# Kernel tuning notes

Hardware: AMD Instinct MI355X
Metric: run time of the kernel (lower is better)

## Reference

```python
import jax, jax.numpy as jnp
import numpy as np
import math

B, SQ, SK = 8, 1024, 1024
DQ = DK = DV = 1024
H = 16
EPS = 1e-5


def _layer_norm(x, g, b):
    mu = jnp.mean(x, axis=-1, keepdims=True)
    var = jnp.mean(jnp.square(x - mu), axis=-1, keepdims=True)
    return (x - mu) * jax.lax.rsqrt(var + EPS) * g + b


def setup_inputs() -> dict:
    key = jax.random.key(0)
    ks = jax.random.split(key, 8)
    s_q = 1.0 / math.sqrt(DQ)
    s_v = 1.0 / math.sqrt(DV)
    return {
        "Q": jax.random.normal(ks[0], (B, SQ, DQ), dtype=jnp.float32),
        "K": jax.random.normal(ks[1], (B, SK, DK), dtype=jnp.float32),
        "Wq": jax.random.normal(ks[2], (DQ, DV), dtype=jnp.float32) * s_q,
        "bq": jnp.zeros((DV,), dtype=jnp.float32),
        "Wk": jax.random.normal(ks[3], (DK, DV), dtype=jnp.float32) * s_q,
        "bk": jnp.zeros((DV,), dtype=jnp.float32),
        "Wv": jax.random.normal(ks[4], (DK, DV), dtype=jnp.float32) * s_q,
        "bv": jnp.zeros((DV,), dtype=jnp.float32),
        "Wo": jax.random.normal(ks[5], (DV, DV), dtype=jnp.float32) * s_v,
        "bo": jnp.zeros((DV,), dtype=jnp.float32),
        "g0": jnp.ones((DV,), dtype=jnp.float32),
        "b0": jnp.zeros((DV,), dtype=jnp.float32),
        "g1": jnp.ones((DV,), dtype=jnp.float32),
        "b1": jnp.zeros((DV,), dtype=jnp.float32),
    }


def reference(Q, K, Wq, bq, Wk, bk, Wv, bv, Wo, bo, g0, b0, g1, b1):
    dh = DV // H
    q = Q @ Wq + bq                      # [B,SQ,DV]
    k = K @ Wk + bk                      # [B,SK,DV]
    v = K @ Wv + bv                      # [B,SK,DV]
    # split/cat over heads == reshape to [B,S,H,dh]
    qh = q.reshape(B, SQ, H, dh)
    kh = k.reshape(B, SK, H, dh)
    vh = v.reshape(B, SK, H, dh)
    # NOTE: original scales by sqrt(dim_V), not sqrt(head_dim)
    scores = jnp.einsum("bqhd,bkhd->bhqk", qh, kh) / math.sqrt(DV)
    A = jax.nn.softmax(scores, axis=-1)  # [B,H,SQ,SK]
    attn = jnp.einsum("bhqk,bkhd->bqhd", A, vh)
    out = q + attn.reshape(B, SQ, DV)    # residual with projected Q
    out = _layer_norm(out, g0, b0)
    out = out + jax.nn.relu(out @ Wo + bo)
    out = _layer_norm(out, g1, b1)
    return out
```

## Files before the change

kernel.cpp:

```cpp
#include <hip/hip_runtime.h>
#include <hip/hip_bf16.h>
#include <stdint.h>

#define NB 8
#define NSQ 1024
#define NSK 1024
#define ND 1024
#define NH 16
#define NDH 64
#define NM (NB * NSQ)
#define LOG2E 1.4426950408889634f

typedef __bf16 bf16;
typedef __bf16 bf16x8 __attribute__((ext_vector_type(8)));
typedef float f32x4 __attribute__((ext_vector_type(4)));
typedef float f32x16 __attribute__((ext_vector_type(16)));
typedef unsigned int uint32;

__device__ __forceinline__ void async_load16(const void* g, void* l) {
  __builtin_amdgcn_global_load_lds(
      (__attribute__((address_space(1))) void*)g,
      (__attribute__((address_space(3))) void*)l, 16, 0, 0);
}

__device__ __forceinline__ void permswap(uint32& x, uint32& y) {
#if __has_builtin(__builtin_amdgcn_permlane32_swap)
  auto r = __builtin_amdgcn_permlane32_swap(x, y, false, false);
  x = r[0]; y = r[1];
#else
  asm volatile("v_permlane32_swap_b32 %0, %1" : "+v"(x), "+v"(y));
#endif
}

__global__ __launch_bounds__(256) void transpose_cvt4(
    const float* __restrict__ W0, const float* __restrict__ W1,
    const float* __restrict__ W2, const float* __restrict__ W3,
    bf16* __restrict__ O0, bf16* __restrict__ O1,
    bf16* __restrict__ O2, bf16* __restrict__ O3) {
  const float* W; bf16* Wt;
  switch (blockIdx.z) {
    case 0: W = W0; Wt = O0; break;
    case 1: W = W1; Wt = O1; break;
    case 2: W = W2; Wt = O2; break;
    default: W = W3; Wt = O3; break;
  }
  __shared__ float t[64][65];
  const int bc = blockIdx.x * 64;
  const int br = blockIdx.y * 64;
  const int tid = threadIdx.x;
  for (int c = tid; c < 1024; c += 256) {
    int r = c >> 4, off = (c & 15) * 4;
    float4 v = *(const float4*)&W[(size_t)(br + r) * 1024 + bc + off];
    t[r][off] = v.x; t[r][off + 1] = v.y; t[r][off + 2] = v.z; t[r][off + 3] = v.w;
  }
  __syncthreads();
  for (int c = tid; c < 512; c += 256) {
    int cc = c >> 3, rr = (c & 7) * 8;
    union { uint4 u; bf16 h[8]; } o;
#pragma unroll
    for (int i = 0; i < 8; ++i) o.h[i] = (bf16)t[rr + i][cc];
    *(uint4*)&Wt[(size_t)(bc + cc) * 1024 + br + rr] = o.u;
  }
}

__global__ __launch_bounds__(256) void transpose_v(const bf16* __restrict__ vsrc,
                                                   bf16* __restrict__ vT) {
  const int st = blockIdx.x * 64;
  const int bh = blockIdx.y;
  const int b = bh >> 4, h = bh & 15;
  __shared__ __align__(16) bf16 t[64][72];
  const int tid = threadIdx.x;
  for (int c = tid; c < 512; c += 256) {
    int s = c >> 3, off = (c & 7) * 8;
    *(uint4*)&t[s][off] =
        *(const uint4*)&vsrc[(size_t)(b * NSK + st + s) * 2048 + 1024 + h * NDH + off];
  }
  __syncthreads();
  for (int c = tid; c < 512; c += 256) {
    int d = c >> 3, s0 = (c & 7) * 8;
    union { uint4 u; bf16 h[8]; } o;
#pragma unroll
    for (int i = 0; i < 8; ++i) o.h[i] = t[s0 + i][d];
    *(uint4*)&vT[((size_t)(bh * NDH + d)) * NSK + st + s0] = o.u;
  }
}

template <int BM, int MODE, int NXC, bool AF32>
__global__ __launch_bounds__(256, 2) void gemm3b(
    const float* __restrict__ Af, const bf16* __restrict__ Ab,
    const bf16* __restrict__ Bt,
    const float* __restrict__ bias, const float* __restrict__ bias2,
    bf16* __restrict__ Cb, const bf16* __restrict__ Resb, float scale, int N) {
  constexpr int NT = 32;
  constexpr int AR = BM / 64;
  constexpr int MR = BM / 32;
  __shared__ __align__(16) bf16 Asl[3][BM * 32];
  __shared__ __align__(16) bf16 Bsl[3][128 * 32];

  const int tid = threadIdx.x;
  const int flat = blockIdx.x;
  const int xi = (flat & 7) * 64 + (flat >> 3);
  const int bcol = (xi & (NXC - 1)) * 128;
  const int brow = (xi / NXC) * BM;

  const int w = tid >> 6, lane = tid & 63;
  const int wm = w >> 1, wn = w & 1;
  const int lr = lane & 15, l4 = lane >> 4;
  const int rgrp = l4 * 4;
  const int gph = (l4 ^ ((lr >> 1) & 3)) * 8;

  const int srow = tid >> 2;
  const int gsrc = (tid & 3) ^ ((tid >> 3) & 3);
  const bf16* Bg = Bt + (size_t)(bcol + srow) * 1024 + gsrc * 8;
  const int ldo = srow * 32 + (tid & 3) * 8;

  auto stageB = [&](int d, int kt) {
#pragma unroll
    for (int r = 0; r < 2; ++r)
      async_load16(Bg + (size_t)r * (64 * 1024) + kt * 32, &Bsl[d][r * 2048 + ldo]);
  };
  auto stageA_lds = [&](int d, int kt) {
#pragma unroll
    for (int r = 0; r < AR; ++r)
      async_load16(Ab + (size_t)(brow + srow + r * 64) * 1024 + gsrc * 8 + kt * 32,
                   &Asl[d][r * 2048 + ldo]);
  };

  float4 areg[AR][2];
  auto issueA = [&](int kt) {
    const float* base = Af + (size_t)(brow + srow) * 1024 + gsrc * 8 + kt * 32;
#pragma unroll
    for (int r = 0; r < AR; ++r) {
      areg[r][0] = *(const float4*)(base + (size_t)r * (64 * 1024));
      areg[r][1] = *(const float4*)(base + (size_t)r * (64 * 1024) + 4);
    }
  };
  auto writeA = [&](int d) {
#pragma unroll
    for (int r = 0; r < AR; ++r) {
      bf16x8 o;
      o[0] = (bf16)areg[r][0].x; o[1] = (bf16)areg[r][0].y;
      o[2] = (bf16)areg[r][0].z; o[3] = (bf16)areg[r][0].w;
      o[4] = (bf16)areg[r][1].x; o[5] = (bf16)areg[r][1].y;
      o[6] = (bf16)areg[r][1].z; o[7] = (bf16)areg[r][1].w;
      *(bf16x8*)&Asl[d][r * 2048 + ldo] = o;
    }
  };
  auto wait_vm_steady = [&]() {
    if constexpr (AF32) {
      if constexpr (BM == 256) asm volatile("s_waitcnt vmcnt(10)" ::: "memory");
      else                     asm volatile("s_waitcnt vmcnt(6)" ::: "memory");
    } else {
      if constexpr (BM == 256) asm volatile("s_waitcnt vmcnt(6)" ::: "memory");
      else                     asm volatile("s_waitcnt vmcnt(4)" ::: "memory");
    }
  };

  f32x4 acc[MR][4] = {};

  if constexpr (AF32) {
    issueA(0); stageB(0, 0);
    writeA(0);
    issueA(1); stageB(1, 1);
    wait_vm_steady();
    asm volatile("s_waitcnt lgkmcnt(0)" ::: "memory");
  } else {
    stageA_lds(0, 0); stageB(0, 0);
    stageA_lds(1, 1); stageB(1, 1);
    wait_vm_steady();
  }
  __builtin_amdgcn_s_barrier();

  int cur = 0, st2 = 2;
  for (int t = 0; t < NT; ++t) {
    bf16x8 af[MR], bfr[4];
#pragma unroll
    for (int i = 0; i < MR; ++i)
      af[i] = *(const bf16x8*)&Asl[cur][(wm * (BM / 2) + i * 16 + lr) * 32 + gph];
#pragma unroll
    for (int n = 0; n < 4; ++n)
      bfr[n] = *(const bf16x8*)&Bsl[cur][(wn * 64 + n * 16 + lr) * 32 + gph];
    if constexpr (AF32) {
      if (t + 1 < NT) writeA((cur == 2) ? 0 : cur + 1);
      if (t + 2 < NT) { issueA(t + 2); stageB(st2, t + 2); }
    } else {
      if (t + 2 < NT) { stageA_lds(st2, t + 2); stageB(st2, t + 2); }
    }
    __builtin_amdgcn_s_setprio(1);
#pragma unroll
    for (int i = 0; i < MR; ++i)
#pragma unroll
      for (int n = 0; n < 4; ++n)
        acc[i][n] = __builtin_amdgcn_mfma_f32_16x16x32_bf16(af[i], bfr[n], acc[i][n], 0, 0, 0);
    __builtin_amdgcn_s_setprio(0);
    if (t + 2 < NT)      wait_vm_steady();
    else if (t + 1 < NT) asm volatile("s_waitcnt vmcnt(0)" ::: "memory");
    asm volatile("s_waitcnt lgkmcnt(0)" ::: "memory");
    __builtin_amdgcn_s_barrier();
    cur = (cur == 2) ? 0 : cur + 1;
    st2 = (st2 == 2) ? 0 : st2 + 1;
  }

#pragma unroll
  for (int m = 0; m < MR; ++m) {
#pragma unroll
    for (int n = 0; n < 4; ++n) {
      const int col = bcol + wn * 64 + n * 16 + lr;
      float bv, sc;
      if (MODE == 2) {
        const bool isV = (bcol >= 1024);
        bv = isV ? bias2[col - 1024] : bias[col];
        sc = isV ? 1.0f : LOG2E;
      } else {
        bv = bias[col];
        sc = scale;
      }
#pragma unroll
      for (int r = 0; r < 4; ++r) {
        const int row = brow + wm * (BM / 2) + m * 16 + rgrp + r;
        float v = acc[m][n][r] + bv;
        if (MODE == 1) {
          float res = (float)Resb[(size_t)row * N + col];
          Cb[(size_t)row * N + col] = (bf16)(res + (v > 0.f ? v : 0.f));
        } else {
          Cb[(size_t)row * N + col] = (bf16)(v * sc);
        }
      }
    }
  }
}

__global__ __launch_bounds__(512, 4) void attn_kernel(
    const bf16* __restrict__ qb, const bf16* __restrict__ kvb,
    const bf16* __restrict__ vT, bf16* __restrict__ attnout) {
  const int bh = blockIdx.y;
  const int b = bh >> 4, h = bh & 15;
  const int tid = threadIdx.x, w = tid >> 6, lane = tid & 63;
  const int l31 = lane & 31;
  const int l1 = lane >> 5;
  const int q0w = blockIdx.x * 256 + w * 32;

  __shared__ __align__(16) bf16 Kl[2][64 * 64];
  __shared__ __align__(16) bf16 Vl[2][64 * 64];

  const int srow = tid >> 3;
  const int sgran = tid & 7;
  const int gsw = sgran ^ (srow & 7);
  const int ldst = srow * 64 + sgran * 8;
  const int rg = l31 & 7;

  const bf16* kbase = kvb + (size_t)(b * NSK) * 2048 + h * NDH;
  const bf16* vbase = vT + (size_t)(bh * NDH) * NSK;

  bf16x8 qf[4];
#pragma unroll
  for (int kd = 0; kd < 4; ++kd)
    qf[kd] = *(const bf16x8*)&qb[(size_t)(b * NSQ + q0w + l31) * ND +
                                 h * NDH + kd * 16 + l1 * 8];

  f32x16 oacc0 = {}, oacc1 = {}, lacc = {};
  bf16x8 ones;
#pragma unroll
  for (int i = 0; i < 8; ++i) ones[i] = (bf16)1.0f;

  auto stage = [&](int bi, int kt) {
    async_load16(kbase + (size_t)(kt + srow) * 2048 + gsw * 8, &Kl[bi][ldst]);
    async_load16(vbase + (size_t)srow * NSK + kt + gsw * 8, &Vl[bi][ldst]);
  };

  stage(0, 0);

  for (int t = 0; t < 16; ++t) {
    const int bi = t & 1;
    asm volatile("s_waitcnt vmcnt(0)" ::: "memory");
    __syncthreads();
    if (t < 15) stage(bi ^ 1, (t + 1) * 64);

    uint32 W[2][4][2];
#pragma unroll
    for (int n = 0; n < 2; ++n) {
      f32x16 s = {};
      __builtin_amdgcn_s_setprio(1);
#pragma unroll
      for (int kd = 0; kd < 4; ++kd) {
        bf16x8 kf = *(const bf16x8*)&Kl[bi][(n * 32 + l31) * 64 + (((kd * 2 + l1) ^ rg) * 8)];
        s = __builtin_amdgcn_mfma_f32_32x32x16_bf16(kf, qf[kd], s, 0, 0, 0);
      }
      __builtin_amdgcn_s_setprio(0);
#pragma unroll
      for (int r2 = 0; r2 < 4; ++r2)
#pragma unroll
        for (int p = 0; p < 2; ++p) {
          float elo = __builtin_amdgcn_exp2f(s[r2 * 4 + 2 * p]);
          float ehi = __builtin_amdgcn_exp2f(s[r2 * 4 + 2 * p + 1]);
          uint32 wd;
          asm("v_cvt_pk_bf16_f32 %0, %1, %2" : "=v"(wd) : "v"(elo), "v"(ehi));
          W[n][r2][p] = wd;
        }
    }
    __builtin_amdgcn_s_setprio(1);
#pragma unroll
    for (int kc = 0; kc < 4; ++kc) {
      uint32 x0 = W[kc >> 1][(kc & 1) * 2][0], y0 = W[kc >> 1][(kc & 1) * 2 + 1][0];
      uint32 x1 = W[kc >> 1][(kc & 1) * 2][1], y1 = W[kc >> 1][(kc & 1) * 2 + 1][1];
      permswap(x0, y0);
      permswap(x1, y1);
      union { uint32 u[4]; bf16x8 v; } cvt;
      cvt.u[0] = x0; cvt.u[1] = x1; cvt.u[2] = y0; cvt.u[3] = y1;
      bf16x8 pa = cvt.v;
      bf16x8 vf0 = *(const bf16x8*)&Vl[bi][(l31) * 64 + (((kc * 2 + l1) ^ rg) * 8)];
      bf16x8 vf1 = *(const bf16x8*)&Vl[bi][(32 + l31) * 64 + (((kc * 2 + l1) ^ rg) * 8)];
      oacc0 = __builtin_amdgcn_mfma_f32_32x32x16_bf16(pa, vf0, oacc0, 0, 0, 0);
      oacc1 = __builtin_amdgcn_mfma_f32_32x32x16_bf16(pa, vf1, oacc1, 0, 0, 0);
      lacc = __builtin_amdgcn_mfma_f32_32x32x16_bf16(pa, ones, lacc, 0, 0, 0);
    }
    __builtin_amdgcn_s_setprio(0);
  }

  float inv[16];
#pragma unroll
  for (int r = 0; r < 16; ++r) inv[r] = 1.0f / lacc[r];
#pragma unroll
  for (int r = 0; r < 16; ++r) {
    const int row = q0w + (r & 3) + 8 * (r >> 2) + 4 * l1;
    attnout[(size_t)(b * NSQ + row) * ND + h * NDH + l31] = (bf16)(oacc0[r] * inv[r]);
    attnout[(size_t)(b * NSQ + row) * ND + h * NDH + 32 + l31] = (bf16)(oacc1[r] * inv[r]);
  }
}

template <bool RES, bool OUTF>
__global__ __launch_bounds__(256) void ln_kernel(
    const bf16* __restrict__ x, const bf16* __restrict__ rq, float rscale,
    const float* __restrict__ g, const float* __restrict__ be,
    bf16* __restrict__ yb, float* __restrict__ yf) {
  __shared__ float sm[4];
  const int row = blockIdx.x, tid = threadIdx.x;
  const size_t base = (size_t)row * ND + tid * 4;
  union { uint2 u; bf16 h[4]; } xv;
  xv.u = *(const uint2*)(x + base);
  float v0 = (float)xv.h[0], v1 = (float)xv.h[1], v2 = (float)xv.h[2], v3 = (float)xv.h[3];
  if (RES) {
    union { uint2 u; bf16 h[4]; } q;
    q.u = *(const uint2*)(rq + base);
    v0 += rscale * (float)q.h[0]; v1 += rscale * (float)q.h[1];
    v2 += rscale * (float)q.h[2]; v3 += rscale * (float)q.h[3];
  }
  float s = v0 + v1 + v2 + v3;
#pragma unroll
  for (int off = 32; off > 0; off >>= 1) s += __shfl_down(s, off, 64);
  if ((tid & 63) == 0) sm[tid >> 6] = s;
  __syncthreads();
  const float mean = (sm[0] + sm[1] + sm[2] + sm[3]) * (1.0f / ND);
  __syncthreads();
  const float d0 = v0 - mean, d1 = v1 - mean, d2 = v2 - mean, d3 = v3 - mean;
  float sq = d0 * d0 + d1 * d1 + d2 * d2 + d3 * d3;
#pragma unroll
  for (int off = 32; off > 0; off >>= 1) sq += __shfl_down(sq, off, 64);
  if ((tid & 63) == 0) sm[tid >> 6] = sq;
  __syncthreads();
  const float var = (sm[0] + sm[1] + sm[2] + sm[3]) * (1.0f / ND);
  const float rs = rsqrtf(var + 1e-5f);
  float4 gv = *(const float4*)(g + tid * 4);
  float4 bv = *(const float4*)(be + tid * 4);
  const float y0 = d0 * rs * gv.x + bv.x;
  const float y1 = d1 * rs * gv.y + bv.y;
  const float y2 = d2 * rs * gv.z + bv.z;
  const float y3 = d3 * rs * gv.w + bv.w;
  if (OUTF) {
    *(float4*)(yf + base) = make_float4(y0, y1, y2, y3);
  } else {
    union { uint2 u; bf16 h[4]; } o;
    o.h[0] = (bf16)y0; o.h[1] = (bf16)y1; o.h[2] = (bf16)y2; o.h[3] = (bf16)y3;
    *(uint2*)(yb + base) = o.u;
  }
}

extern "C" void kernel_launch(void* const* d_in, const int* in_sizes, int n_in,
                              void* d_out, int out_size, void* d_ws, size_t ws_size,
                              hipStream_t stream) {
  const float* Q  = (const float*)d_in[0];
  const float* K  = (const float*)d_in[1];
  const float* Wq = (const float*)d_in[2];
  const float* bq = (const float*)d_in[3];
  const float* Wk = (const float*)d_in[4];
  const float* bk = (const float*)d_in[5];
  const float* Wv = (const float*)d_in[6];
  const float* bv = (const float*)d_in[7];
  const float* Wo = (const float*)d_in[8];
  const float* bo = (const float*)d_in[9];
  const float* g0 = (const float*)d_in[10];
  const float* b0 = (const float*)d_in[11];
  const float* g1 = (const float*)d_in[12];
  const float* b1 = (const float*)d_in[13];
  float* out = (float*)d_out;

  char* ws = (char*)d_ws;
  const size_t MB = 1024 * 1024;
  bf16* Wqt   = (bf16*)(ws + 32 * MB);
  bf16* Wkvt  = (bf16*)(ws + 34 * MB);
  bf16* Wot   = (bf16*)(ws + 38 * MB);
  bf16* qb    = (bf16*)(ws + 40 * MB);
  bf16* kvb   = (bf16*)(ws + 56 * MB);
  bf16* vT    = (bf16*)(ws + 88 * MB);
  bf16* attnb = (bf16*)(ws + 104 * MB);
  bf16* h0b   = (bf16*)(ws + 56 * MB);
  bf16* out1b = (bf16*)(ws + 0);

  transpose_cvt4<<<dim3(16, 16, 4), 256, 0, stream>>>(
      Wq, Wk, Wv, Wo, Wqt, Wkvt, Wkvt + 1024 * 1024, Wot);
  gemm3b<256, 2, 16, true><<<512, 256, 0, stream>>>(K, nullptr, Wkvt, bk, bv, kvb, nullptr, 1.0f, 2048);
  gemm3b<128, 0, 8, true><<<512, 256, 0, stream>>>(Q, nullptr, Wqt, bq, nullptr, qb, nullptr, 0.03125f, 1024);
  transpose_v<<<dim3(16, 128), 256, 0, stream>>>(kvb, vT);
  attn_kernel<<<dim3(4, 128), 512, 0, stream>>>(qb, kvb, vT, attnb);
  ln_kernel<true, false><<<8192, 256, 0, stream>>>(attnb, qb, 32.0f, g0, b0, h0b, nullptr);
  gemm3b<128, 1, 8, false><<<512, 256, 0, stream>>>(nullptr, h0b, Wot, bo, nullptr, out1b, h0b, 1.0f, 1024);
  ln_kernel<false, true><<<8192, 256, 0, stream>>>(out1b, nullptr, 0.f, g1, b1, nullptr, out);
}
```

Measured before the change: 174.6 us.

## Triple-buffer attention K/V, pre-convert K to bf16, move residual into LayerNorm

The attention kernel moves from double to triple-buffered K/V shared memory. The next-next tile is issued mid-iteration, with a partial vmcnt wait and a single barrier per iteration, so loads overlap compute better. K is converted to bf16 in a separate kernel so the KV projection GEMM reads bf16 instead of converting fp32 in its main loop. The output GEMM no longer reads the residual; the final LayerNorm adds h0 instead, which removes one read in the GEMM epilogue but adds an extra conversion pass over K and more LDS per block.

```diff
diff --git a/kernel.cpp b/kernel.cpp
--- a/kernel.cpp
+++ b/kernel.cpp
@@ -30,6 +30,15 @@
 #else
   asm volatile("v_permlane32_swap_b32 %0, %1" : "+v"(x), "+v"(y));
 #endif
+}
+
+__global__ __launch_bounds__(256) void cvt1_f32_bf16(const float* __restrict__ in,
+                                                     bf16* __restrict__ out) {
+  int i = blockIdx.x * 256 + threadIdx.x;
+  float4 v = *(const float4*)(in + (size_t)i * 4);
+  union { uint64_t u; bf16 h[4]; } o;
+  o.h[0] = (bf16)v.x; o.h[1] = (bf16)v.y; o.h[2] = (bf16)v.z; o.h[3] = (bf16)v.w;
+  *(uint64_t*)(out + (size_t)i * 4) = o.u;
 }
 
 __global__ __launch_bounds__(256) void transpose_cvt4(
@@ -90,7 +99,7 @@
     const float* __restrict__ Af, const bf16* __restrict__ Ab,
     const bf16* __restrict__ Bt,
     const float* __restrict__ bias, const float* __restrict__ bias2,
-    bf16* __restrict__ Cb, const bf16* __restrict__ Resb, float scale, int N) {
+    bf16* __restrict__ Cb, float scale, int N) {
   constexpr int NT = 32;
   constexpr int AR = BM / 64;
   constexpr int MR = BM / 32;
@@ -220,8 +229,7 @@
         const int row = brow + wm * (BM / 2) + m * 16 + rgrp + r;
         float v = acc[m][n][r] + bv;
         if (MODE == 1) {
-          float res = (float)Resb[(size_t)row * N + col];
-          Cb[(size_t)row * N + col] = (bf16)(res + (v > 0.f ? v : 0.f));
+          Cb[(size_t)row * N + col] = (bf16)(v > 0.f ? v : 0.f);
         } else {
           Cb[(size_t)row * N + col] = (bf16)(v * sc);
         }
@@ -240,8 +248,8 @@
   const int l1 = lane >> 5;
   const int q0w = blockIdx.x * 256 + w * 32;
 
-  __shared__ __align__(16) bf16 Kl[2][64 * 64];
-  __shared__ __align__(16) bf16 Vl[2][64 * 64];
+  __shared__ __align__(16) bf16 Kl[3][64 * 64];
+  __shared__ __align__(16) bf16 Vl[3][64 * 64];
 
   const int srow = tid >> 3;
   const int sgran = tid & 7;
@@ -269,13 +277,12 @@
   };
 
   stage(0, 0);
-
+  stage(1, 64);
+  asm volatile("s_waitcnt vmcnt(2)" ::: "memory");
+  __builtin_amdgcn_s_barrier();
+
+  int cur = 0, st2 = 2;
   for (int t = 0; t < 16; ++t) {
-    const int bi = t & 1;
-    asm volatile("s_waitcnt vmcnt(0)" ::: "memory");
-    __syncthreads();
-    if (t < 15) stage(bi ^ 1, (t + 1) * 64);
-
     uint32 W[2][4][2];
 #pragma unroll
     for (int n = 0; n < 2; ++n) {
@@ -283,7 +290,7 @@
       __builtin_amdgcn_s_setprio(1);
 #pragma unroll
       for (int kd = 0; kd < 4; ++kd) {
-        bf16x8 kf = *(const bf16x8*)&Kl[bi][(n * 32 + l31) * 64 + (((kd * 2 + l1) ^ rg) * 8)];
+        bf16x8 kf = *(const bf16x8*)&Kl[cur][(n * 32 + l31) * 64 + (((kd * 2 + l1) ^ rg) * 8)];
         s = __builtin_amdgcn_mfma_f32_32x32x16_bf16(kf, qf[kd], s, 0, 0, 0);
       }
       __builtin_amdgcn_s_setprio(0);
@@ -298,6 +305,7 @@
           W[n][r2][p] = wd;
         }
     }
+    if (t + 2 < 16) stage(st2, (t + 2) * 64);
     __builtin_amdgcn_s_setprio(1);
 #pragma unroll
     for (int kc = 0; kc < 4; ++kc) {
@@ -308,13 +316,19 @@
       union { uint32 u[4]; bf16x8 v; } cvt;
       cvt.u[0] = x0; cvt.u[1] = x1; cvt.u[2] = y0; cvt.u[3] = y1;
       bf16x8 pa = cvt.v;
-      bf16x8 vf0 = *(const bf16x8*)&Vl[bi][(l31) * 64 + (((kc * 2 + l1) ^ rg) * 8)];
-      bf16x8 vf1 = *(const bf16x8*)&Vl[bi][(32 + l31) * 64 + (((kc * 2 + l1) ^ rg) * 8)];
+      bf16x8 vf0 = *(const bf16x8*)&Vl[cur][(l31) * 64 + (((kc * 2 + l1) ^ rg) * 8)];
+      bf16x8 vf1 = *(const bf16x8*)&Vl[cur][(32 + l31) * 64 + (((kc * 2 + l1) ^ rg) * 8)];
       oacc0 = __builtin_amdgcn_mfma_f32_32x32x16_bf16(pa, vf0, oacc0, 0, 0, 0);
       oacc1 = __builtin_amdgcn_mfma_f32_32x32x16_bf16(pa, vf1, oacc1, 0, 0, 0);
       lacc = __builtin_amdgcn_mfma_f32_32x32x16_bf16(pa, ones, lacc, 0, 0, 0);
     }
     __builtin_amdgcn_s_setprio(0);
+    if (t + 2 < 16)      asm volatile("s_waitcnt vmcnt(2)" ::: "memory");
+    else if (t + 1 < 16) asm volatile("s_waitcnt vmcnt(0)" ::: "memory");
+    asm volatile("s_waitcnt lgkmcnt(0)" ::: "memory");
+    __builtin_amdgcn_s_barrier();
+    cur = (cur == 2) ? 0 : cur + 1;
+    st2 = (st2 == 2) ? 0 : st2 + 1;
   }
 
   float inv[16];
@@ -396,6 +410,7 @@
 
   char* ws = (char*)d_ws;
   const size_t MB = 1024 * 1024;
+  bf16* Kb    = (bf16*)(ws + 0);
   bf16* Wqt   = (bf16*)(ws + 32 * MB);
   bf16* Wkvt  = (bf16*)(ws + 34 * MB);
   bf16* Wot   = (bf16*)(ws + 38 * MB);
@@ -404,15 +419,16 @@
   bf16* vT    = (bf16*)(ws + 88 * MB);
   bf16* attnb = (bf16*)(ws + 104 * MB);
   bf16* h0b   = (bf16*)(ws + 56 * MB);
-  bf16* out1b = (bf16*)(ws + 0);
+  bf16* relub = (bf16*)(ws + 0);
 
   transpose_cvt4<<<dim3(16, 16, 4), 256, 0, stream>>>(
       Wq, Wk, Wv, Wo, Wqt, Wkvt, Wkvt + 1024 * 1024, Wot);
-  gemm3b<256, 2, 16, true><<<512, 256, 0, stream>>>(K, nullptr, Wkvt, bk, bv, kvb, nullptr, 1.0f, 2048);
-  gemm3b<128, 0, 8, true><<<512, 256, 0, stream>>>(Q, nullptr, Wqt, bq, nullptr, qb, nullptr, 0.03125f, 1024);
+  cvt1_f32_bf16<<<8192, 256, 0, stream>>>(K, Kb);
+  gemm3b<256, 2, 16, false><<<512, 256, 0, stream>>>(nullptr, Kb, Wkvt, bk, bv, kvb, 1.0f, 2048);
+  gemm3b<128, 0, 8, true><<<512, 256, 0, stream>>>(Q, nullptr, Wqt, bq, nullptr, qb, 0.03125f, 1024);
   transpose_v<<<dim3(16, 128), 256, 0, stream>>>(kvb, vT);
   attn_kernel<<<dim3(4, 128), 512, 0, stream>>>(qb, kvb, vT, attnb);
   ln_kernel<true, false><<<8192, 256, 0, stream>>>(attnb, qb, 32.0f, g0, b0, h0b, nullptr);
-  gemm3b<128, 1, 8, false><<<512, 256, 0, stream>>>(nullptr, h0b, Wot, bo, nullptr, out1b, h0b, 1.0f, 1024);
-  ln_kernel<false, true><<<8192, 256, 0, stream>>>(out1b, nullptr, 0.f, g1, b1, nullptr, out);
-}
+  gemm3b<128, 1, 8, false><<<512, 256, 0, stream>>>(nullptr, h0b, Wot, bo, nullptr, relub, 1.0f, 1024);
+  ln_kernel<true, true><<<8192, 256, 0, stream>>>(relub, h0b, 1.0f, g1, b1, nullptr, out);
+}
```

Result: slower. 178.7 us (+2.3%).
